# Optimization experiments

Measured on AMD Instinct MI355X. Metric: run time of the kernel, lower is better.

Reference implementation:

```python
import jax, jax.numpy as jnp
import numpy as np

OUTLINER_RATIO = 0.01
SUB_OUTLINER_BIT = 8
NEG_INF = -1e9


def setup_inputs() -> dict:
    key = jax.random.key(0)
    T, H, D = 4096, 8, 64
    qkv = jax.random.normal(key, (T, 3, H, D), dtype=jnp.float32)
    cu_seqlens = jnp.array([0, 1024, 2048, 3072, 4096], dtype=jnp.int32)
    return {"qkv": qkv, "cu_seqlens": cu_seqlens, "max_seqlen": 1024}


def _varlen_attention(q, k, v, cu_seqlens, causal=False):
    # q,k,v: [T, H, D]; sequences delimited by cu_seqlens (attention never
    # crosses segment boundaries, matching flash_attn_varlen semantics).
    T, H, D = q.shape
    scale = D ** (-0.5)
    pos = jnp.arange(T)
    seg = jnp.searchsorted(cu_seqlens, pos, side="right") - 1  # [T] segment ids
    mask = seg[:, None] == seg[None, :]                          # [T, T]
    if causal:
        mask = mask & (pos[:, None] >= pos[None, :])
    scores = jnp.einsum("thd,shd->hts", q, k) * scale            # [H, T, T]
    scores = jnp.where(mask[None, :, :], scores, NEG_INF)
    probs = jax.nn.softmax(scores, axis=-1)
    out = jnp.einsum("hts,shd->thd", probs, v)                   # [T, H, D]
    return out


def _outlier_quant_compress(x, outliner_ratio=OUTLINER_RATIO, bit=SUB_OUTLINER_BIT):
    # Outlier detection: keep top-ratio |x| entries in full precision;
    # quantize the residual (sub-outliers) to `bit` bits per-tensor.
    a = jnp.abs(x)
    thr = jnp.quantile(a.reshape(-1), 1.0 - outliner_ratio)
    outliers = jnp.where(a > thr, x, 0.0)
    resid = x - outliers
    qmax = 2.0 ** (bit - 1) - 1.0
    scale = jnp.maximum(jnp.max(jnp.abs(resid)), 1e-8) / qmax
    q = jnp.clip(jnp.round(resid / scale), -qmax, qmax)
    x_hat = outliers + q * scale  # decompressed approximation
    return x_hat, thr, scale


def reference(qkv, cu_seqlens, max_seqlen):
    q, k, v = qkv[:, 0], qkv[:, 1], qkv[:, 2]
    out = _varlen_attention(q, k, v, cu_seqlens, causal=False)
    # Compression pipeline (stats + quantize) runs on Q,K,V,O in the original
    # forward; it does not alter the forward output.
    for t in (q, k, v, out):
        _outlier_quant_compress(t)
    return out
```

## Files before the change

### kernel.cpp

```cpp
#include <hip/hip_runtime.h>


#define HEADS 8
#define DH 64
#define TQ 64
#define TK 64
#define KSTR 72
#define NEG_BIG -1e30f
#define L2E 1.44269504088896340736f

using f32x4 = __attribute__((ext_vector_type(4))) float;
using s16x8 = __attribute__((ext_vector_type(8))) short;
using u16x4 = __attribute__((ext_vector_type(4))) unsigned short;

__device__ inline unsigned short bf16b(float x) {
    union { float f; unsigned u; } c; c.f = x;
    unsigned r = c.u + 0x7fffu + ((c.u >> 16) & 1u);
    return (unsigned short)(r >> 16);
}
__device__ inline unsigned pk2(float a, float b) {
    return (unsigned)bf16b(a) | ((unsigned)bf16b(b) << 16);
}

__global__ __launch_bounds__(256, 4)
void fa_mfma_kernel(const float* __restrict__ qkv, const int* __restrict__ cu,
                    int n_cu, int T, float* __restrict__ out,
                    float* __restrict__ Opart, float* __restrict__ Mp,
                    float* __restrict__ Lp) {
    __shared__ unsigned short Ksh[TK][KSTR];
    __shared__ unsigned short Vt[DH][KSTR];
    __shared__ unsigned short Psh[TQ][KSTR];

    const int tid   = threadIdx.x;
    const int h     = blockIdx.y;
    const int t0    = blockIdx.x * TQ;
    const int split = blockIdx.z;
    const int nsplit = gridDim.z;
    const int w    = tid >> 6;
    const int lane = tid & 63;
    const int n15  = lane & 15;
    const int quad = lane >> 4;
    const int c4   = tid & 15;
    const int r0   = tid >> 4;

    int trow = t0 + w * 16 + n15;
    if (trow > T - 1) trow = T - 1;
    int lo, hi;
    {
        int s = 0;
        for (int j = 1; j < n_cu - 1; ++j) if (cu[j] <= trow) s = j;
        lo = cu[s]; hi = cu[s + 1];
    }
    int kb, ke;
    {
        int s = 0;
        for (int j = 1; j < n_cu - 1; ++j) if (cu[j] <= t0) s = j;
        kb = cu[s];
        int tl = t0 + TQ - 1; if (tl > T - 1) tl = T - 1;
        s = 0;
        for (int j = 1; j < n_cu - 1; ++j) if (cu[j] <= tl) s = j;
        ke = cu[s + 1];
    }

    s16x8 qfrag[2];
    {
        int tq = t0 + w * 16 + n15;
        int tc = tq < T ? tq : T - 1;
        const float* qp = qkv + (((size_t)tc * 3 + 0) * HEADS + h) * DH + quad * 8;
        #pragma unroll
        for (int kh = 0; kh < 2; ++kh) {
            float4 x = *(const float4*)(qp + kh * 32);
            float4 y = *(const float4*)(qp + kh * 32 + 4);
            s16x8 f;
            f[0] = (short)bf16b(x.x * 0.125f); f[1] = (short)bf16b(x.y * 0.125f);
            f[2] = (short)bf16b(x.z * 0.125f); f[3] = (short)bf16b(x.w * 0.125f);
            f[4] = (short)bf16b(y.x * 0.125f); f[5] = (short)bf16b(y.y * 0.125f);
            f[6] = (short)bf16b(y.z * 0.125f); f[7] = (short)bf16b(y.w * 0.125f);
            qfrag[kh] = f;
        }
    }

    f32x4 oacc[4];
    #pragma unroll
    for (int i = 0; i < 4; ++i) oacc[i] = (f32x4){0.f, 0.f, 0.f, 0.f};
    float m_ = NEG_BIG, l_ = 0.f;

    const int c0_start = (kb / TK) * TK + split * TK;

    for (int c0 = c0_start; c0 < ke; c0 += nsplit * TK) {
        #pragma unroll
        for (int rr = 0; rr < TK; rr += 16) {
            int krow = rr + r0;
            int kk = c0 + krow;
            float4 v = make_float4(0.f, 0.f, 0.f, 0.f);
            if (kk < T)
                v = *(const float4*)(qkv + (((size_t)kk * 3 + 1) * HEADS + h) * DH + 4 * c4);
            u16x4 p; p[0] = bf16b(v.x); p[1] = bf16b(v.y); p[2] = bf16b(v.z); p[3] = bf16b(v.w);
            *(u16x4*)&Ksh[krow][4 * c4] = p;
        }
        #pragma unroll
        for (int it = 0; it < 2; ++it) {
            int r2 = 2 * (r0 + 16 * it);
            int ka = c0 + r2;
            float4 va = make_float4(0.f, 0.f, 0.f, 0.f);
            float4 vb = make_float4(0.f, 0.f, 0.f, 0.f);
            if (ka < T)
                va = *(const float4*)(qkv + (((size_t)ka * 3 + 2) * HEADS + h) * DH + 4 * c4);
            if (ka + 1 < T)
                vb = *(const float4*)(qkv + (((size_t)(ka + 1) * 3 + 2) * HEADS + h) * DH + 4 * c4);
            const float* pa = &va.x; const float* pb = &vb.x;
            #pragma unroll
            for (int i = 0; i < 4; ++i) {
                unsigned pk = (unsigned)bf16b(pa[i]) | ((unsigned)bf16b(pb[i]) << 16);
                *(unsigned*)&Vt[4 * c4 + i][r2] = pk;
            }
        }
        __syncthreads();

        f32x4 sacc[4];
        #pragma unroll
        for (int nt = 0; nt < 4; ++nt) sacc[nt] = (f32x4){0.f, 0.f, 0.f, 0.f};
        #pragma unroll
        for (int nt = 0; nt < 4; ++nt) {
            #pragma unroll
            for (int kh = 0; kh < 2; ++kh) {
                s16x8 kfr = *(const s16x8*)&Ksh[nt * 16 + n15][kh * 32 + quad * 8];
                sacc[nt] = __builtin_amdgcn_mfma_f32_16x16x32_bf16(kfr, qfrag[kh], sacc[nt], 0, 0, 0);
            }
        }

        if (!(c0 >= lo && c0 + TK <= hi)) {
            #pragma unroll
            for (int nt = 0; nt < 4; ++nt)
                #pragma unroll
                for (int reg = 0; reg < 4; ++reg) {
                    int key = c0 + nt * 16 + quad * 4 + reg;
                    bool valid = (key >= lo) && (key < hi);
                    sacc[nt][reg] = valid ? sacc[nt][reg] : NEG_BIG;
                }
        }

        float rm = NEG_BIG;
        #pragma unroll
        for (int nt = 0; nt < 4; ++nt)
            #pragma unroll
            for (int reg = 0; reg < 4; ++reg) rm = fmaxf(rm, sacc[nt][reg]);
        rm = fmaxf(rm, __shfl_xor(rm, 16));
        rm = fmaxf(rm, __shfl_xor(rm, 32));
        float mn = fmaxf(m_, rm);
        float alpha = exp2f((m_ - mn) * L2E);
        float mnl = mn * L2E;
        float rs = 0.f;
        #pragma unroll
        for (int nt = 0; nt < 4; ++nt) {
            float p0 = exp2f(fmaf(sacc[nt][0], L2E, -mnl));
            float p1 = exp2f(fmaf(sacc[nt][1], L2E, -mnl));
            float p2 = exp2f(fmaf(sacc[nt][2], L2E, -mnl));
            float p3 = exp2f(fmaf(sacc[nt][3], L2E, -mnl));
            rs += (p0 + p1) + (p2 + p3);
            *(uint2*)&Psh[w * 16 + n15][nt * 16 + quad * 4] =
                make_uint2(pk2(p0, p1), pk2(p2, p3));
        }
        rs += __shfl_xor(rs, 16);
        rs += __shfl_xor(rs, 32);
        l_ = fmaf(l_, alpha, rs);
        m_ = mn;
        #pragma unroll
        for (int reg = 0; reg < 4; ++reg) {
            float ar = __shfl(alpha, quad * 4 + reg);
            oacc[0][reg] *= ar; oacc[1][reg] *= ar;
            oacc[2][reg] *= ar; oacc[3][reg] *= ar;
        }

        s16x8 afr[2];
        #pragma unroll
        for (int kh = 0; kh < 2; ++kh)
            afr[kh] = *(const s16x8*)&Psh[w * 16 + n15][kh * 32 + quad * 8];
        #pragma unroll
        for (int nt = 0; nt < 4; ++nt) {
            #pragma unroll
            for (int kh = 0; kh < 2; ++kh) {
                s16x8 vfr = *(const s16x8*)&Vt[nt * 16 + n15][kh * 32 + quad * 8];
                oacc[nt] = __builtin_amdgcn_mfma_f32_16x16x32_bf16(afr[kh], vfr, oacc[nt], 0, 0, 0);
            }
        }
        __syncthreads();
    }

    if (nsplit == 1) {
        #pragma unroll
        for (int reg = 0; reg < 4; ++reg) {
            float lr = __shfl(l_, quad * 4 + reg);
            float inv = 1.f / fmaxf(lr, 1e-30f);
            int t = t0 + w * 16 + quad * 4 + reg;
            if (t < T) {
                #pragma unroll
                for (int nt = 0; nt < 4; ++nt)
                    out[((size_t)t * HEADS + h) * DH + nt * 16 + n15] = oacc[nt][reg] * inv;
            }
        }
    } else {
        #pragma unroll
        for (int reg = 0; reg < 4; ++reg) {
            int t = t0 + w * 16 + quad * 4 + reg;
            if (t < T) {
                size_t base = (((size_t)split * T + t) * HEADS + h) * DH;
                #pragma unroll
                for (int nt = 0; nt < 4; ++nt)
                    Opart[base + nt * 16 + n15] = oacc[nt][reg];
            }
        }
        int tq = t0 + w * 16 + n15;
        if (quad == 0 && tq < T) {
            size_t mi = ((size_t)split * T + tq) * HEADS + h;
            Mp[mi] = m_; Lp[mi] = l_;
        }
    }
}

__global__ __launch_bounds__(256)
void fa_combine_kernel(const float* __restrict__ Opart, const float* __restrict__ Mp,
                       const float* __restrict__ Lp, float* __restrict__ out, int T) {
    int i4 = blockIdx.x * blockDim.x + threadIdx.x;
    int total = T * HEADS * (DH / 4);
    if (i4 >= total) return;
    int th = i4 / (DH / 4);
    int d4 = i4 - th * (DH / 4);
    size_t stride = (size_t)T * HEADS * DH;
    int mlstride = T * HEADS;
    float m0 = Mp[th], m1 = Mp[mlstride + th];
    float l0 = Lp[th], l1 = Lp[mlstride + th];
    float M = fmaxf(m0, m1);
    float w0 = exp2f((m0 - M) * L2E);
    float w1 = exp2f((m1 - M) * L2E);
    float L = fmaxf(fmaf(l0, w0, l1 * w1), 1e-30f);
    float inv = 1.f / L;
    size_t off = (size_t)th * DH + 4 * d4;
    float4 a = *(const float4*)&Opart[off];
    float4 b = *(const float4*)&Opart[stride + off];
    float4 o;
    o.x = fmaf(a.x, w0, b.x * w1) * inv;
    o.y = fmaf(a.y, w0, b.y * w1) * inv;
    o.z = fmaf(a.z, w0, b.z * w1) * inv;
    o.w = fmaf(a.w, w0, b.w * w1) * inv;
    *(float4*)&out[off] = o;
}

extern "C" void kernel_launch(void* const* d_in, const int* in_sizes, int n_in,
                              void* d_out, int out_size, void* d_ws, size_t ws_size,
                              hipStream_t stream) {
    const float* qkv = (const float*)d_in[0];
    const int* cu    = (const int*)d_in[1];
    const int n_cu   = in_sizes[1];
    const int T      = in_sizes[0] / (3 * HEADS * DH);
    float* out       = (float*)d_out;

    const int NSPLIT = 2;
    size_t need = (size_t)NSPLIT * T * HEADS * DH * sizeof(float)
                + 2 * (size_t)NSPLIT * T * HEADS * sizeof(float);

    if (ws_size >= need) {
        float* Opart = (float*)d_ws;
        float* Mpp   = Opart + (size_t)NSPLIT * T * HEADS * DH;
        float* Lpp   = Mpp + (size_t)NSPLIT * T * HEADS;
        dim3 grid(T / TQ, HEADS, NSPLIT);
        fa_mfma_kernel<<<grid, 256, 0, stream>>>(qkv, cu, n_cu, T, out, Opart, Mpp, Lpp);
        int total4 = T * HEADS * (DH / 4);
        fa_combine_kernel<<<(total4 + 255) / 256, 256, 0, stream>>>(Opart, Mpp, Lpp, out, T);
    } else {
        dim3 grid(T / TQ, HEADS, 1);
        fa_mfma_kernel<<<grid, 256, 0, stream>>>(qkv, cu, n_cu, T, out,
                                                 (float*)d_ws, (float*)d_ws, (float*)d_ws);
    }
}
```

Measured before the change: 114.3 us.

## Pre-convert QKV to bf16 layouts and stream K/V tiles via direct-to-LDS loads

Adds a prep kernel that converts Q (pre-scaled), K (head-major) and V (transposed) to bf16 once, instead of every attention block re-reading fp32 QKV and converting it per tile. The main kernel then fills XOR-swizzled LDS tiles with global_load_lds and reads MFMA fragments through swizzled offsets, which removes the per-thread conversion and the bank-conflicting stores. It also uses a hardware packed bf16 convert when available. The cost is an extra kernel launch and an extra pass over QKV. The fallback path for a small workspace is gone, so the code now assumes the workspace always fits.

```diff
diff --git a/kernel.cpp b/kernel.cpp
--- a/kernel.cpp
+++ b/kernel.cpp
@@ -5,128 +5,167 @@
 #define DH 64
 #define TQ 64
 #define TK 64
-#define KSTR 72
+#define PSTR 72
 #define NEG_BIG -1e30f
 #define L2E 1.44269504088896340736f
 
 using f32x4 = __attribute__((ext_vector_type(4))) float;
 using s16x8 = __attribute__((ext_vector_type(8))) short;
-using u16x4 = __attribute__((ext_vector_type(4))) unsigned short;
 
 __device__ inline unsigned short bf16b(float x) {
     union { float f; unsigned u; } c; c.f = x;
     unsigned r = c.u + 0x7fffu + ((c.u >> 16) & 1u);
     return (unsigned short)(r >> 16);
 }
+
+#if __has_builtin(__builtin_amdgcn_cvt_pk_bf16_f32)
+__device__ inline unsigned pk2(float a, float b) {
+    auto v = __builtin_amdgcn_cvt_pk_bf16_f32(a, b);
+    unsigned u; __builtin_memcpy(&u, &v, 4); return u;
+}
+#else
 __device__ inline unsigned pk2(float a, float b) {
     return (unsigned)bf16b(a) | ((unsigned)bf16b(b) << 16);
 }
+#endif
+
+__global__ __launch_bounds__(256)
+void prep_kernel(const float* __restrict__ qkv, unsigned short* __restrict__ Qb,
+                 unsigned short* __restrict__ Kb, unsigned short* __restrict__ Vtb,
+                 int T) {
+    __shared__ unsigned short Lt[64][PSTR];
+    const int m = blockIdx.z, h = blockIdx.y, t0 = blockIdx.x * 64;
+    const int tid = threadIdx.x, d8 = tid & 7, tr = tid >> 3;
+
+    #pragma unroll
+    for (int i = 0; i < 2; ++i) {
+        int t = t0 + i * 32 + tr;
+        int tc = t < T ? t : T - 1;
+        const float* src = qkv + ((size_t)tc * 3 + m) * (HEADS * DH) + h * DH + d8 * 8;
+        float4 a = *(const float4*)src;
+        float4 b = *(const float4*)(src + 4);
+        if (m == 0) {
+            a.x *= 0.125f; a.y *= 0.125f; a.z *= 0.125f; a.w *= 0.125f;
+            b.x *= 0.125f; b.y *= 0.125f; b.z *= 0.125f; b.w *= 0.125f;
+        }
+        unsigned p0 = pk2(a.x, a.y), p1 = pk2(a.z, a.w);
+        unsigned p2 = pk2(b.x, b.y), p3 = pk2(b.z, b.w);
+        if (m == 2) {
+            *(uint2*)&Lt[i * 32 + tr][d8 * 8]     = make_uint2(p0, p1);
+            *(uint2*)&Lt[i * 32 + tr][d8 * 8 + 4] = make_uint2(p2, p3);
+        } else if (t < T) {
+            unsigned short* dst = (m == 0)
+                ? (Qb + (size_t)t * (HEADS * DH) + h * DH + d8 * 8)
+                : (Kb + ((size_t)h * T + t) * DH + d8 * 8);
+            *(uint4*)dst = make_uint4(p0, p1, p2, p3);
+        }
+    }
+    if (m == 2) {
+        __syncthreads();
+        const int d = tid >> 2, tg = tid & 3;
+        #pragma unroll
+        for (int p = 0; p < 2; ++p) {
+            int G = tg + 4 * p;
+            int td = t0 + G * 8;
+            unsigned u[4];
+            #pragma unroll
+            for (int jj = 0; jj < 4; ++jj)
+                u[jj] = (unsigned)Lt[G * 8 + 2 * jj][d] |
+                        ((unsigned)Lt[G * 8 + 2 * jj + 1][d] << 16);
+            if (td < T)
+                *(uint4*)(Vtb + ((size_t)h * DH + d) * T + td) =
+                    make_uint4(u[0], u[1], u[2], u[3]);
+        }
+    }
+}
 
 __global__ __launch_bounds__(256, 4)
-void fa_mfma_kernel(const float* __restrict__ qkv, const int* __restrict__ cu,
-                    int n_cu, int T, float* __restrict__ out,
-                    float* __restrict__ Opart, float* __restrict__ Mp,
-                    float* __restrict__ Lp) {
-    __shared__ unsigned short Ksh[TK][KSTR];
-    __shared__ unsigned short Vt[DH][KSTR];
-    __shared__ unsigned short Psh[TQ][KSTR];
-
-    const int tid   = threadIdx.x;
-    const int h     = blockIdx.y;
-    const int t0    = blockIdx.x * TQ;
-    const int split = blockIdx.z;
-    const int nsplit = gridDim.z;
-    const int w    = tid >> 6;
-    const int lane = tid & 63;
-    const int n15  = lane & 15;
-    const int quad = lane >> 4;
-    const int c4   = tid & 15;
-    const int r0   = tid >> 4;
-
-    int trow = t0 + w * 16 + n15;
-    if (trow > T - 1) trow = T - 1;
+void fa_main(const unsigned short* __restrict__ Qb, const unsigned short* __restrict__ Kb,
+             const unsigned short* __restrict__ Vtb, const int* __restrict__ cu,
+             int n_cu, int T, float* __restrict__ out,
+             float* __restrict__ Opart, float* __restrict__ Mp, float* __restrict__ Lp) {
+    __shared__ unsigned short Ksh[TK * DH];
+    __shared__ unsigned short Vsh[DH * TK];
+    __shared__ unsigned short Psh[TQ][PSTR];
+
+    const int tid = threadIdx.x;
+    const int h = blockIdx.y, t0 = blockIdx.x * TQ;
+    const int split = blockIdx.z, nsplit = gridDim.z;
+    const int w = tid >> 6, lane = tid & 63, n15 = lane & 15, quad = lane >> 4;
+
+    int trow = t0 + w * 16 + n15; if (trow > T - 1) trow = T - 1;
     int lo, hi;
-    {
-        int s = 0;
-        for (int j = 1; j < n_cu - 1; ++j) if (cu[j] <= trow) s = j;
-        lo = cu[s]; hi = cu[s + 1];
-    }
-    int kb, ke;
-    {
-        int s = 0;
-        for (int j = 1; j < n_cu - 1; ++j) if (cu[j] <= t0) s = j;
-        kb = cu[s];
-        int tl = t0 + TQ - 1; if (tl > T - 1) tl = T - 1;
-        s = 0;
-        for (int j = 1; j < n_cu - 1; ++j) if (cu[j] <= tl) s = j;
-        ke = cu[s + 1];
-    }
+    { int s = 0; for (int j = 1; j < n_cu - 1; ++j) if (cu[j] <= trow) s = j;
+      lo = cu[s]; hi = cu[s + 1]; }
+    int kb_, ke;
+    { int s = 0; for (int j = 1; j < n_cu - 1; ++j) if (cu[j] <= t0) s = j;
+      kb_ = cu[s];
+      int tl = t0 + TQ - 1; if (tl > T - 1) tl = T - 1;
+      s = 0; for (int j = 1; j < n_cu - 1; ++j) if (cu[j] <= tl) s = j;
+      ke = cu[s + 1]; }
 
     s16x8 qfrag[2];
     {
-        int tq = t0 + w * 16 + n15;
-        int tc = tq < T ? tq : T - 1;
-        const float* qp = qkv + (((size_t)tc * 3 + 0) * HEADS + h) * DH + quad * 8;
-        #pragma unroll
-        for (int kh = 0; kh < 2; ++kh) {
-            float4 x = *(const float4*)(qp + kh * 32);
-            float4 y = *(const float4*)(qp + kh * 32 + 4);
-            s16x8 f;
-            f[0] = (short)bf16b(x.x * 0.125f); f[1] = (short)bf16b(x.y * 0.125f);
-            f[2] = (short)bf16b(x.z * 0.125f); f[3] = (short)bf16b(x.w * 0.125f);
-            f[4] = (short)bf16b(y.x * 0.125f); f[5] = (short)bf16b(y.y * 0.125f);
-            f[6] = (short)bf16b(y.z * 0.125f); f[7] = (short)bf16b(y.w * 0.125f);
-            qfrag[kh] = f;
-        }
-    }
+        int tc = t0 + w * 16 + n15; if (tc > T - 1) tc = T - 1;
+        const unsigned short* qp = Qb + (size_t)tc * (HEADS * DH) + h * DH + quad * 8;
+        qfrag[0] = *(const s16x8*)qp;
+        qfrag[1] = *(const s16x8*)(qp + 32);
+    }
+
+    const unsigned short* kb_h = Kb + (size_t)h * T * DH;
+    const unsigned short* vt_h = Vtb + (size_t)h * DH * T;
+    int krow_rel[2], vkey_off[2];
+    const unsigned short* kbase[2];
+    const unsigned short* vbase[2];
+    #pragma unroll
+    for (int i = 0; i < 2; ++i) {
+        int gg = i * 64 + lane;
+        int rr = gg >> 3;
+        int gc = gg & 7;
+        int row = w * 16 + rr;
+        int gcol = gc ^ (row & 7);
+        krow_rel[i] = row;
+        kbase[i] = kb_h + gcol * 8;
+        vbase[i] = vt_h + (size_t)row * T;
+        vkey_off[i] = gcol * 8;
+    }
+    int off16[2];
+    #pragma unroll
+    for (int kh = 0; kh < 2; ++kh)
+        off16[kh] = n15 * 128 + (((kh * 4 + quad) ^ (n15 & 7)) * 16);
 
     f32x4 oacc[4];
     #pragma unroll
     for (int i = 0; i < 4; ++i) oacc[i] = (f32x4){0.f, 0.f, 0.f, 0.f};
     float m_ = NEG_BIG, l_ = 0.f;
 
-    const int c0_start = (kb / TK) * TK + split * TK;
-
+    const int c0_start = (kb_ / TK) * TK + split * TK;
     for (int c0 = c0_start; c0 < ke; c0 += nsplit * TK) {
         #pragma unroll
-        for (int rr = 0; rr < TK; rr += 16) {
-            int krow = rr + r0;
-            int kk = c0 + krow;
-            float4 v = make_float4(0.f, 0.f, 0.f, 0.f);
-            if (kk < T)
-                v = *(const float4*)(qkv + (((size_t)kk * 3 + 1) * HEADS + h) * DH + 4 * c4);
-            u16x4 p; p[0] = bf16b(v.x); p[1] = bf16b(v.y); p[2] = bf16b(v.z); p[3] = bf16b(v.w);
-            *(u16x4*)&Ksh[krow][4 * c4] = p;
-        }
-        #pragma unroll
-        for (int it = 0; it < 2; ++it) {
-            int r2 = 2 * (r0 + 16 * it);
-            int ka = c0 + r2;
-            float4 va = make_float4(0.f, 0.f, 0.f, 0.f);
-            float4 vb = make_float4(0.f, 0.f, 0.f, 0.f);
-            if (ka < T)
-                va = *(const float4*)(qkv + (((size_t)ka * 3 + 2) * HEADS + h) * DH + 4 * c4);
-            if (ka + 1 < T)
-                vb = *(const float4*)(qkv + (((size_t)(ka + 1) * 3 + 2) * HEADS + h) * DH + 4 * c4);
-            const float* pa = &va.x; const float* pb = &vb.x;
-            #pragma unroll
-            for (int i = 0; i < 4; ++i) {
-                unsigned pk = (unsigned)bf16b(pa[i]) | ((unsigned)bf16b(pb[i]) << 16);
-                *(unsigned*)&Vt[4 * c4 + i][r2] = pk;
-            }
+        for (int i = 0; i < 2; ++i) {
+            int rk = c0 + krow_rel[i]; if (rk > T - 1) rk = T - 1;
+            __builtin_amdgcn_global_load_lds(
+                (const __attribute__((address_space(1))) void*)(kbase[i] + ((size_t)rk << 6)),
+                (__attribute__((address_space(3))) void*)&Ksh[(w * 128 + i * 64) * 8],
+                16, 0, 0);
+            int kv = c0 + vkey_off[i]; if (kv > T - 8) kv = T - 8;
+            __builtin_amdgcn_global_load_lds(
+                (const __attribute__((address_space(1))) void*)(vbase[i] + kv),
+                (__attribute__((address_space(3))) void*)&Vsh[(w * 128 + i * 64) * 8],
+                16, 0, 0);
         }
         __syncthreads();
 
+        const char* Kc = (const char*)Ksh;
         f32x4 sacc[4];
         #pragma unroll
-        for (int nt = 0; nt < 4; ++nt) sacc[nt] = (f32x4){0.f, 0.f, 0.f, 0.f};
-        #pragma unroll
         for (int nt = 0; nt < 4; ++nt) {
-            #pragma unroll
-            for (int kh = 0; kh < 2; ++kh) {
-                s16x8 kfr = *(const s16x8*)&Ksh[nt * 16 + n15][kh * 32 + quad * 8];
-                sacc[nt] = __builtin_amdgcn_mfma_f32_16x16x32_bf16(kfr, qfrag[kh], sacc[nt], 0, 0, 0);
-            }
+            s16x8 k0 = *(const s16x8*)(Kc + nt * 2048 + off16[0]);
+            s16x8 k1 = *(const s16x8*)(Kc + nt * 2048 + off16[1]);
+            f32x4 z = (f32x4){0.f, 0.f, 0.f, 0.f};
+            z = __builtin_amdgcn_mfma_f32_16x16x32_bf16(k0, qfrag[0], z, 0, 0, 0);
+            z = __builtin_amdgcn_mfma_f32_16x16x32_bf16(k1, qfrag[1], z, 0, 0, 0);
+            sacc[nt] = z;
         }
 
         if (!(c0 >= lo && c0 + TK <= hi)) {
@@ -173,16 +212,15 @@
         }
 
         s16x8 afr[2];
-        #pragma unroll
-        for (int kh = 0; kh < 2; ++kh)
-            afr[kh] = *(const s16x8*)&Psh[w * 16 + n15][kh * 32 + quad * 8];
+        afr[0] = *(const s16x8*)&Psh[w * 16 + n15][quad * 8];
+        afr[1] = *(const s16x8*)&Psh[w * 16 + n15][32 + quad * 8];
+        const char* Vc = (const char*)Vsh;
         #pragma unroll
         for (int nt = 0; nt < 4; ++nt) {
-            #pragma unroll
-            for (int kh = 0; kh < 2; ++kh) {
-                s16x8 vfr = *(const s16x8*)&Vt[nt * 16 + n15][kh * 32 + quad * 8];
-                oacc[nt] = __builtin_amdgcn_mfma_f32_16x16x32_bf16(afr[kh], vfr, oacc[nt], 0, 0, 0);
-            }
+            s16x8 v0 = *(const s16x8*)(Vc + nt * 2048 + off16[0]);
+            s16x8 v1 = *(const s16x8*)(Vc + nt * 2048 + off16[1]);
+            oacc[nt] = __builtin_amdgcn_mfma_f32_16x16x32_bf16(afr[0], v0, oacc[nt], 0, 0, 0);
+            oacc[nt] = __builtin_amdgcn_mfma_f32_16x16x32_bf16(afr[1], v1, oacc[nt], 0, 0, 0);
         }
         __syncthreads();
     }
@@ -256,20 +294,22 @@
     float* out       = (float*)d_out;
 
     const int NSPLIT = 2;
-    size_t need = (size_t)NSPLIT * T * HEADS * DH * sizeof(float)
-                + 2 * (size_t)NSPLIT * T * HEADS * sizeof(float);
-
-    if (ws_size >= need) {
-        float* Opart = (float*)d_ws;
-        float* Mpp   = Opart + (size_t)NSPLIT * T * HEADS * DH;
-        float* Lpp   = Mpp + (size_t)NSPLIT * T * HEADS;
-        dim3 grid(T / TQ, HEADS, NSPLIT);
-        fa_mfma_kernel<<<grid, 256, 0, stream>>>(qkv, cu, n_cu, T, out, Opart, Mpp, Lpp);
-        int total4 = T * HEADS * (DH / 4);
-        fa_combine_kernel<<<(total4 + 255) / 256, 256, 0, stream>>>(Opart, Mpp, Lpp, out, T);
-    } else {
-        dim3 grid(T / TQ, HEADS, 1);
-        fa_mfma_kernel<<<grid, 256, 0, stream>>>(qkv, cu, n_cu, T, out,
-                                                 (float*)d_ws, (float*)d_ws, (float*)d_ws);
-    }
-}
+    size_t elems = (size_t)T * HEADS * DH;
+
+    float* Opart = (float*)d_ws;
+    float* Mpp   = Opart + (size_t)NSPLIT * elems;
+    float* Lpp   = Mpp + (size_t)NSPLIT * T * HEADS;
+    unsigned short* Qb  = (unsigned short*)(Lpp + (size_t)NSPLIT * T * HEADS);
+    unsigned short* Kb  = Qb + elems;
+    unsigned short* Vtb = Kb + elems;
+
+    int tiles = (T + TQ - 1) / TQ;
+    dim3 pgrid(tiles, HEADS, 3);
+    prep_kernel<<<pgrid, 256, 0, stream>>>(qkv, Qb, Kb, Vtb, T);
+
+    dim3 grid(tiles, HEADS, NSPLIT);
+    fa_main<<<grid, 256, 0, stream>>>(Qb, Kb, Vtb, cu, n_cu, T, out, Opart, Mpp, Lpp);
+
+    int total4 = T * HEADS * (DH / 4);
+    fa_combine_kernel<<<(total4 + 255) / 256, 256, 0, stream>>>(Opart, Mpp, Lpp, out, T);
+}
```

New measurement: 105.9 us. -7.3%, faster.
